# Kernel optimization log

Measured on AMD Instinct MI355X. Metric: run time of the kernel, lower is better.

## Reference

```python
import jax, jax.numpy as jnp
import numpy as np


def _avgpool2(x):
    # 2x2 average pool, stride 2, NHWC
    B, H, W, C = x.shape
    return x.reshape(B, H // 2, 2, W // 2, 2, C).mean(axis=(2, 4))


def setup_inputs() -> dict:
    key = jax.random.key(0)
    ks = jax.random.split(key, 5)
    B, H, W, C = 8, 64, 64, 512
    s = 0.02
    return {
        "x": jax.random.normal(ks[0], (B, H, W, C), dtype=jnp.float32),
        "wf": jax.random.normal(ks[1], (C, C // 8), dtype=jnp.float32) * s,
        "wg": jax.random.normal(ks[2], (C, C // 8), dtype=jnp.float32) * s,
        "wh": jax.random.normal(ks[3], (C, C // 2), dtype=jnp.float32) * s,
        "wo": jax.random.normal(ks[4], (C // 2, C), dtype=jnp.float32) * s,
    }


def reference(x, wf, wg, wh, wo):
    B, H, W, C = x.shape
    # queries from full resolution: 1x1 conv == channel matmul
    f = jnp.einsum("bhwc,cd->bhwd", x, wf).reshape(B, H * W, C // 8)
    # keys/values from 2x2 average-pooled map
    xp = _avgpool2(x)  # [B, H/2, W/2, C]
    g = jnp.einsum("bhwc,cd->bhwd", xp, wg).reshape(B, H * W // 4, C // 8)
    h = jnp.einsum("bhwc,cd->bhwd", xp, wh).reshape(B, H * W // 4, C // 2)
    # attn: [B, HW, HW/4], softmax over pooled key axis
    attn = jax.nn.softmax(jnp.einsum("bnd,bmd->bnm", f, g), axis=-1)
    y = jnp.einsum("bnm,bmd->bnd", attn, h).reshape(B, H, W, C // 2)
    # output 1x1 conv back to C channels
    return jnp.einsum("bhwc,cd->bhwd", y, wo)
```

## Files before the change

kernel.cpp:

```cpp
#include <hip/hip_runtime.h>
#include <hip/hip_bf16.h>

typedef __attribute__((ext_vector_type(8))) short bshort8;
typedef __attribute__((ext_vector_type(4))) float f32x4;
typedef __attribute__((ext_vector_type(4))) float vfloat4;
typedef __attribute__((ext_vector_type(4))) unsigned int vuint4;
typedef __attribute__((ext_vector_type(2))) unsigned int vuint2;

__device__ __forceinline__ unsigned short f2bf(float f) {
    union { float f; unsigned u; } v; v.f = f;
    unsigned u = v.u;
    u += 0x7fffu + ((u >> 16) & 1u);
    return (unsigned short)(u >> 16);
}

template<int EPI>
__global__ __launch_bounds__(256)
void gemm_bt(const unsigned short* __restrict__ Av, const unsigned short* __restrict__ Btv,
             void* __restrict__ Cv,
             int M, int N, int K,
             long long aB, long long bB, long long cB)
{
    __shared__ __align__(128) char sA[64 * 64];
    __shared__ __align__(128) char sB[64 * 64];

    const int b    = blockIdx.z;
    const int tid  = threadIdx.x;
    const int bRow = blockIdx.y << 6;
    const int bCol = blockIdx.x << 6;
    const int wid  = tid >> 6, lane = tid & 63;
    const int wr   = wid >> 1, wc   = wid & 1;
    const int r16  = lane & 15, kg  = lane >> 4;
    const int srow = tid >> 2,  skc = tid & 3;

    const unsigned short* A  = Av  + (size_t)aB * b;
    const unsigned short* Bt = Btv + (size_t)bB * b;

    f32x4 acc[2][2] = {};

    const size_t aRowBase = (size_t)(bRow + srow) * K + skc * 8;
    const size_t bRowBase = (size_t)(bCol + srow) * K + skc * 8;
    const unsigned swW = ((((unsigned)srow) << 6) | (((unsigned)skc) << 4))
                         ^ ((((unsigned)srow) & 7u) << 4);

    for (int k0 = 0; k0 < K; k0 += 32) {
        vuint4 apack = *(const vuint4*)(A  + aRowBase + k0);
        vuint4 bpack = *(const vuint4*)(Bt + bRowBase + k0);
        *(vuint4*)(sA + swW) = apack;
        *(vuint4*)(sB + swW) = bpack;
        __syncthreads();

        bshort8 af[2], bfr[2];
        #pragma unroll
        for (int mi = 0; mi < 2; mi++) {
            unsigned row = (unsigned)(wr * 32 + mi * 16 + r16);
            unsigned off = ((row << 6) | (((unsigned)kg) << 4)) ^ ((row & 7u) << 4);
            af[mi] = *(const bshort8*)(sA + off);
        }
        #pragma unroll
        for (int ni = 0; ni < 2; ni++) {
            unsigned col = (unsigned)(wc * 32 + ni * 16 + r16);
            unsigned off = ((col << 6) | (((unsigned)kg) << 4)) ^ ((col & 7u) << 4);
            bfr[ni] = *(const bshort8*)(sB + off);
        }
        #pragma unroll
        for (int mi = 0; mi < 2; mi++)
            #pragma unroll
            for (int ni = 0; ni < 2; ni++)
                acc[mi][ni] = __builtin_amdgcn_mfma_f32_16x16x32_bf16(
                                  af[mi], bfr[ni], acc[mi][ni], 0, 0, 0);
        __syncthreads();
    }

    #pragma unroll
    for (int mi = 0; mi < 2; mi++) {
        const int row0 = bRow + wr * 32 + mi * 16 + kg * 4;
        #pragma unroll
        for (int ni = 0; ni < 2; ni++) {
            const int col = bCol + wc * 32 + ni * 16 + r16;
            #pragma unroll
            for (int r = 0; r < 4; r++) {
                const int row = row0 + r;
                float x = acc[mi][ni][r];
                const size_t ci = (size_t)cB * b + (size_t)row * N + col;
                if constexpr (EPI == 0) ((float*)Cv)[ci] = x;
                else                    ((unsigned short*)Cv)[ci] = f2bf(x);
            }
        }
    }
}

__global__ __launch_bounds__(512)
void flash_attn(const float* __restrict__ x,
                const unsigned short* __restrict__ wft,
                const unsigned short* __restrict__ gb,
                const unsigned short* __restrict__ ht,
                unsigned short* __restrict__ yb)
{
    __shared__ __align__(128) char sS[128 * 128];
    __shared__ __align__(128) char sG[2][64 * 128];
    __shared__ __align__(128) char sH[2][256 * 128];
    __shared__ float rs[128];

    const int tid = threadIdx.x;
    const int bid = blockIdx.x;
    const int b   = bid & 7;
    const int q0  = (bid >> 3) << 7;
    const int wid = tid >> 6, lane = tid & 63;
    const int wr  = wid >> 1, wc = wid & 1;
    const int r16 = lane & 15, kg = lane >> 4;

    const float*          xB = x  + ((size_t)b * 4096 + q0) * 512;
    const unsigned short* gB = gb + (size_t)b * 1024 * 64;
    const unsigned short* hB = ht + (size_t)b * 256 * 1024;

    char* const sG0 = sG[0];
    char* const sH0 = sH[0];

    f32x4 facc[4] = {};
    {
        const int xrow = tid >> 2, xc = tid & 3;
        const int wrow = tid >> 3, wkc = tid & 7;
        const int frow = wid << 4;
        for (int k0 = 0; k0 < 512; k0 += 64) {
            {
                const float* p = xB + (size_t)xrow * 512 + k0 + xc * 16;
                #pragma unroll
                for (int j = 0; j < 2; j++) {
                    vfloat4 a0 = *(const vfloat4*)(p + j * 8);
                    vfloat4 a1 = *(const vfloat4*)(p + j * 8 + 4);
                    vuint4 w;
                    w[0] = (unsigned)f2bf(a0[0]) | ((unsigned)f2bf(a0[1]) << 16);
                    w[1] = (unsigned)f2bf(a0[2]) | ((unsigned)f2bf(a0[3]) << 16);
                    w[2] = (unsigned)f2bf(a1[0]) | ((unsigned)f2bf(a1[1]) << 16);
                    w[3] = (unsigned)f2bf(a1[2]) | ((unsigned)f2bf(a1[3]) << 16);
                    unsigned off = ((unsigned)xrow * 128 + (unsigned)(xc * 32 + j * 16))
                                   ^ (((unsigned)xrow & 7u) << 4);
                    *(vuint4*)(sH0 + off) = w;
                }
            }
            {
                vuint4 v = *(const vuint4*)(wft + (size_t)wrow * 512 + k0 + wkc * 8);
                unsigned off = ((unsigned)wrow * 128 + (unsigned)wkc * 16)
                               ^ (((unsigned)wrow & 7u) << 4);
                *(vuint4*)(sG0 + off) = v;
            }
            __syncthreads();

            bshort8 ax[2];
            {
                unsigned row = (unsigned)(frow + r16);
                unsigned base = row * 128, sw = (row & 7u) << 4;
                ax[0] = *(const bshort8*)(sH0 + ((base + (unsigned)kg * 16) ^ sw));
                ax[1] = *(const bshort8*)(sH0 + ((base + 64 + (unsigned)kg * 16) ^ sw));
            }
            #pragma unroll
            for (int ni = 0; ni < 4; ni++) {
                unsigned col = (unsigned)(ni * 16 + r16);
                unsigned base = col * 128, sw = (col & 7u) << 4;
                bshort8 b0 = *(const bshort8*)(sG0 + ((base + (unsigned)kg * 16) ^ sw));
                bshort8 b1 = *(const bshort8*)(sG0 + ((base + 64 + (unsigned)kg * 16) ^ sw));
                facc[ni] = __builtin_amdgcn_mfma_f32_16x16x32_bf16(ax[0], b0, facc[ni], 0, 0, 0);
                facc[ni] = __builtin_amdgcn_mfma_f32_16x16x32_bf16(ax[1], b1, facc[ni], 0, 0, 0);
            }
            __syncthreads();
        }

        const int frow2 = wid << 4;
        #pragma unroll
        for (int ni = 0; ni < 4; ni++) {
            const unsigned col = (unsigned)(ni * 16 + r16);
            #pragma unroll
            for (int r = 0; r < 4; r++) {
                unsigned row = (unsigned)(frow2 + kg * 4 + r);
                unsigned off = (row * 128 + col * 2) ^ ((row & 7u) << 4);
                *(unsigned short*)(sS + off) = f2bf(facc[ni][r]);
            }
        }
    }

    const int kc = tid & 7, n0 = tid >> 3;
    const unsigned gOff  = ((unsigned)n0 * 128 + (unsigned)kc * 16) ^ (((unsigned)n0 & 7u) << 4);
    const unsigned hOff0 = gOff;

    vuint4 gR, hR0, hR1, hR2, hR3;
    gR  = *(const vuint4*)(gB + (size_t)n0 * 64 + kc * 8);
    hR0 = *(const vuint4*)(hB + (size_t)(n0      ) * 1024 + kc * 8);
    hR1 = *(const vuint4*)(hB + (size_t)(n0 +  64) * 1024 + kc * 8);
    hR2 = *(const vuint4*)(hB + (size_t)(n0 + 128) * 1024 + kc * 8);
    hR3 = *(const vuint4*)(hB + (size_t)(n0 + 192) * 1024 + kc * 8);
    *(vuint4*)(sG0 + gOff)               = gR;
    *(vuint4*)(sH0 + hOff0)              = hR0;
    *(vuint4*)(sH0 + hOff0 +     8192)   = hR1;
    *(vuint4*)(sH0 + hOff0 + 2 * 8192)   = hR2;
    *(vuint4*)(sH0 + hOff0 + 3 * 8192)   = hR3;
    __syncthreads();

    bshort8 af[2][2];
    #pragma unroll
    for (int mi = 0; mi < 2; mi++) {
        unsigned row = (unsigned)(wr * 32 + mi * 16 + r16);
        unsigned base = row * 128, sw = (row & 7u) << 4;
        af[mi][0] = *(const bshort8*)(sS + ((base + (unsigned)kg * 16) ^ sw));
        af[mi][1] = *(const bshort8*)(sS + ((base + 64 + (unsigned)kg * 16) ^ sw));
    }
    __syncthreads();

    f32x4 yacc[2][8] = {};
    float psum[2][4] = {};

    for (int c = 0; c < 16; c++) {
        const int cur = c & 1;
        char* const sGc = sG[cur];
        char* const sHc = sH[cur];

        if (c < 15) {
            const int kv1 = (c + 1) << 6;
            gR  = *(const vuint4*)(gB + (size_t)(kv1 + n0) * 64 + kc * 8);
            hR0 = *(const vuint4*)(hB + (size_t)(n0      ) * 1024 + kv1 + kc * 8);
            hR1 = *(const vuint4*)(hB + (size_t)(n0 +  64) * 1024 + kv1 + kc * 8);
            hR2 = *(const vuint4*)(hB + (size_t)(n0 + 128) * 1024 + kv1 + kc * 8);
            hR3 = *(const vuint4*)(hB + (size_t)(n0 + 192) * 1024 + kv1 + kc * 8);
        }

        f32x4 sacc[2][2] = {};
        #pragma unroll
        for (int ni = 0; ni < 2; ni++) {
            unsigned col = (unsigned)(wc * 32 + ni * 16 + r16);
            unsigned base = col * 128, sw = (col & 7u) << 4;
            bshort8 g0 = *(const bshort8*)(sGc + ((base + (unsigned)kg * 16) ^ sw));
            bshort8 g1 = *(const bshort8*)(sGc + ((base + 64 + (unsigned)kg * 16) ^ sw));
            #pragma unroll
            for (int mi = 0; mi < 2; mi++) {
                sacc[mi][ni] = __builtin_amdgcn_mfma_f32_16x16x32_bf16(af[mi][0], g0, sacc[mi][ni], 0, 0, 0);
                sacc[mi][ni] = __builtin_amdgcn_mfma_f32_16x16x32_bf16(af[mi][1], g1, sacc[mi][ni], 0, 0, 0);
            }
        }

        #pragma unroll
        for (int mi = 0; mi < 2; mi++)
            #pragma unroll
            for (int ni = 0; ni < 2; ni++) {
                const unsigned col = (unsigned)(wc * 32 + ni * 16 + r16);
                #pragma unroll
                for (int r = 0; r < 4; r++) {
                    float e = __expf(sacc[mi][ni][r]);
                    psum[mi][r] += e;
                    unsigned row = (unsigned)(wr * 32 + mi * 16 + kg * 4 + r);
                    unsigned off = (row * 128 + col * 2) ^ ((row & 7u) << 4);
                    *(unsigned short*)(sS + off) = f2bf(e);
                }
            }
        __syncthreads();

        bshort8 pa[2][2];
        #pragma unroll
        for (int mi = 0; mi < 2; mi++) {
            unsigned row = (unsigned)(wr * 32 + mi * 16 + r16);
            unsigned base = row * 128, sw = (row & 7u) << 4;
            pa[mi][0] = *(const bshort8*)(sS + ((base + (unsigned)kg * 16) ^ sw));
            pa[mi][1] = *(const bshort8*)(sS + ((base + 64 + (unsigned)kg * 16) ^ sw));
        }
        #pragma unroll
        for (int ni = 0; ni < 8; ni++) {
            unsigned col = (unsigned)(wc * 128 + ni * 16 + r16);
            unsigned base = col * 128, sw = (col & 7u) << 4;
            bshort8 b0 = *(const bshort8*)(sHc + ((base + (unsigned)kg * 16) ^ sw));
            bshort8 b1 = *(const bshort8*)(sHc + ((base + 64 + (unsigned)kg * 16) ^ sw));
            #pragma unroll
            for (int mi = 0; mi < 2; mi++) {
                yacc[mi][ni] = __builtin_amdgcn_mfma_f32_16x16x32_bf16(pa[mi][0], b0, yacc[mi][ni], 0, 0, 0);
                yacc[mi][ni] = __builtin_amdgcn_mfma_f32_16x16x32_bf16(pa[mi][1], b1, yacc[mi][ni], 0, 0, 0);
            }
        }

        if (c < 15) {
            char* const sGn = sG[cur ^ 1];
            char* const sHn = sH[cur ^ 1];
            *(vuint4*)(sGn + gOff)             = gR;
            *(vuint4*)(sHn + hOff0)            = hR0;
            *(vuint4*)(sHn + hOff0 +     8192) = hR1;
            *(vuint4*)(sHn + hOff0 + 2 * 8192) = hR2;
            *(vuint4*)(sHn + hOff0 + 3 * 8192) = hR3;
        }
        __syncthreads();
    }

    #pragma unroll
    for (int mi = 0; mi < 2; mi++)
        #pragma unroll
        for (int r = 0; r < 4; r++) {
            float s = psum[mi][r];
            s += __shfl_xor(s, 1, 64);
            s += __shfl_xor(s, 2, 64);
            s += __shfl_xor(s, 4, 64);
            s += __shfl_xor(s, 8, 64);
            psum[mi][r] = s;
        }
    if (wc == 0 && r16 == 0) {
        #pragma unroll
        for (int mi = 0; mi < 2; mi++)
            #pragma unroll
            for (int r = 0; r < 4; r++)
                rs[wr * 32 + mi * 16 + kg * 4 + r] = psum[mi][r];
    }
    __syncthreads();
    if (wc == 1 && r16 == 0) {
        #pragma unroll
        for (int mi = 0; mi < 2; mi++)
            #pragma unroll
            for (int r = 0; r < 4; r++)
                rs[wr * 32 + mi * 16 + kg * 4 + r] += psum[mi][r];
    }
    __syncthreads();

    unsigned short* yB = yb + ((size_t)b * 4096 + q0) * 256;
    #pragma unroll
    for (int mi = 0; mi < 2; mi++)
        #pragma unroll
        for (int r = 0; r < 4; r++) {
            const int row = wr * 32 + mi * 16 + kg * 4 + r;
            const float rinv = 1.0f / rs[row];
            #pragma unroll
            for (int ni = 0; ni < 8; ni++) {
                const int col = wc * 128 + ni * 16 + r16;
                yB[(size_t)row * 256 + col] = f2bf(yacc[mi][ni][r] * rinv);
            }
        }
}

__global__ __launch_bounds__(256)
void pool2(const float* __restrict__ x, unsigned short* __restrict__ xp)
{
    const int t  = blockIdx.x * 256 + threadIdx.x;
    const int c4 = t & 127;
    const int j  = (t >> 7) & 31;
    const int i  = (t >> 12) & 31;
    const int b  = t >> 17;
    const float* p = x + ((((size_t)b * 64 + 2 * i) * 64) + 2 * j) * 512 + c4 * 4;
    vfloat4 a0 = *(const vfloat4*)p;
    vfloat4 a1 = *(const vfloat4*)(p + 512);
    vfloat4 a2 = *(const vfloat4*)(p + 64 * 512);
    vfloat4 a3 = *(const vfloat4*)(p + 64 * 512 + 512);
    float r0 = 0.25f * (a0[0] + a1[0] + a2[0] + a3[0]);
    float r1 = 0.25f * (a0[1] + a1[1] + a2[1] + a3[1]);
    float r2 = 0.25f * (a0[2] + a1[2] + a2[2] + a3[2]);
    float r3 = 0.25f * (a0[3] + a1[3] + a2[3] + a3[3]);
    vuint2 o;
    o[0] = (unsigned)f2bf(r0) | ((unsigned)f2bf(r1) << 16);
    o[1] = (unsigned)f2bf(r2) | ((unsigned)f2bf(r3) << 16);
    *(vuint2*)(xp + (size_t)t * 4) = o;
}

__global__ __launch_bounds__(256)
void wprep(const float* __restrict__ wf, const float* __restrict__ wg,
           const float* __restrict__ wh, const float* __restrict__ wo,
           unsigned short* __restrict__ wf_t, unsigned short* __restrict__ wg_t,
           unsigned short* __restrict__ wh_t, unsigned short* __restrict__ wo_t)
{
    __shared__ float tile[32][33];
    int t = blockIdx.x;
    const float* in; unsigned short* out; int K, N;
    if (t < 32)       { in = wf; out = wf_t; K = 512; N = 64;  }
    else if (t < 64)  { in = wg; out = wg_t; K = 512; N = 64;  t -= 32;  }
    else if (t < 192) { in = wh; out = wh_t; K = 512; N = 256; t -= 64;  }
    else              { in = wo; out = wo_t; K = 256; N = 512; t -= 192; }
    const int ntN = N >> 5;
    const int tk = (t / ntN) << 5, tn = (t % ntN) << 5;
    const int tx = threadIdx.x & 31, ty = threadIdx.x >> 5;
    #pragma unroll
    for (int s = 0; s < 4; s++)
        tile[ty + s * 8][tx] = in[(size_t)(tk + ty + s * 8) * N + tn + tx];
    __syncthreads();
    #pragma unroll
    for (int s = 0; s < 4; s++)
        out[(size_t)(tn + ty + s * 8) * K + tk + tx] = f2bf(tile[tx][ty + s * 8]);
}

extern "C" void kernel_launch(void* const* d_in, const int* in_sizes, int n_in,
                              void* d_out, int out_size, void* d_ws, size_t ws_size,
                              hipStream_t stream)
{
    const float* x  = (const float*)d_in[0];
    const float* wf = (const float*)d_in[1];
    const float* wg = (const float*)d_in[2];
    const float* wh = (const float*)d_in[3];
    const float* wo = (const float*)d_in[4];
    float* out = (float*)d_out;

    char* ws = (char*)d_ws;
    size_t off = 0;
    auto carve = [&](size_t bytes) {
        char* p = ws + off;
        off = (off + bytes + 255) & ~(size_t)255;
        return p;
    };
    unsigned short* xp   = (unsigned short*)carve(8ll * 1024 * 512 * 2);
    unsigned short* wf_t = (unsigned short*)carve(64 * 512 * 2);
    unsigned short* wg_t = (unsigned short*)carve(64 * 512 * 2);
    unsigned short* wh_t = (unsigned short*)carve(256 * 512 * 2);
    unsigned short* wo_t = (unsigned short*)carve(512 * 256 * 2);
    unsigned short* gb   = (unsigned short*)carve(8ll * 1024 * 64 * 2);
    unsigned short* ht   = (unsigned short*)carve(8ll * 256 * 1024 * 2);
    unsigned short* yb   = (unsigned short*)carve(8ll * 4096 * 256 * 2);

    wprep<<<dim3(320), 256, 0, stream>>>(wf, wg, wh, wo, wf_t, wg_t, wh_t, wo_t);

    pool2<<<dim3(4096), 256, 0, stream>>>(x, xp);

    gemm_bt<1><<<dim3(1, 128, 1), 256, 0, stream>>>(xp, wg_t, gb, 8192, 64, 512, 0, 0, 0);
    gemm_bt<1><<<dim3(16, 4, 8), 256, 0, stream>>>(wh_t, xp, ht, 256, 1024, 512,
                                                   0, 1024LL * 512, 256LL * 1024);

    flash_attn<<<dim3(256), 512, 0, stream>>>(x, wf_t, gb, ht, yb);

    gemm_bt<0><<<dim3(8, 512, 1), 256, 0, stream>>>(yb, wo_t, out, 32768, 512, 256, 0, 0, 0);
}
```

Before: 203.3 us.

## Give each wave its own 16 query rows to drop intra-loop barriers

Each of the 8 waves now owns 16 full query rows instead of a 32x(half-key/half-value) tile. The score matrix is computed transposed (G as the A operand), so the exp'd probabilities land in per-wave LDS scratch that only that wave reads. This removes one block-wide barrier per KV chunk and the cross-wave row-sum reduction through shared memory. It also adds s_setprio around MFMA sections. In exchange each wave reads all 256 H columns from LDS and holds 16 accumulators, which raises LDS traffic for B fragments and register pressure.

```diff
diff --git a/kernel.cpp b/kernel.cpp
--- a/kernel.cpp
+++ b/kernel.cpp
@@ -100,14 +100,12 @@
     __shared__ __align__(128) char sS[128 * 128];
     __shared__ __align__(128) char sG[2][64 * 128];
     __shared__ __align__(128) char sH[2][256 * 128];
-    __shared__ float rs[128];
 
     const int tid = threadIdx.x;
     const int bid = blockIdx.x;
     const int b   = bid & 7;
     const int q0  = (bid >> 3) << 7;
     const int wid = tid >> 6, lane = tid & 63;
-    const int wr  = wid >> 1, wc = wid & 1;
     const int r16 = lane & 15, kg = lane >> 4;
 
     const float*          xB = x  + ((size_t)b * 4096 + q0) * 512;
@@ -196,18 +194,16 @@
     *(vuint4*)(sH0 + hOff0 + 3 * 8192)   = hR3;
     __syncthreads();
 
-    bshort8 af[2][2];
-    #pragma unroll
-    for (int mi = 0; mi < 2; mi++) {
-        unsigned row = (unsigned)(wr * 32 + mi * 16 + r16);
-        unsigned base = row * 128, sw = (row & 7u) << 4;
-        af[mi][0] = *(const bshort8*)(sS + ((base + (unsigned)kg * 16) ^ sw));
-        af[mi][1] = *(const bshort8*)(sS + ((base + 64 + (unsigned)kg * 16) ^ sw));
-    }
-    __syncthreads();
-
-    f32x4 yacc[2][8] = {};
-    float psum[2][4] = {};
+    char* const sP = sS + (wid << 11);
+    bshort8 af[2];
+    {
+        unsigned base = (unsigned)r16 * 128, sw = ((unsigned)r16 & 7u) << 4;
+        af[0] = *(const bshort8*)(sP + ((base + (unsigned)kg * 16) ^ sw));
+        af[1] = *(const bshort8*)(sP + ((base + 64 + (unsigned)kg * 16) ^ sw));
+    }
+
+    f32x4 yacc[16] = {};
+    float psum = 0.f;
 
     for (int c = 0; c < 16; c++) {
         const int cur = c & 1;
@@ -223,56 +219,53 @@
             hR3 = *(const vuint4*)(hB + (size_t)(n0 + 192) * 1024 + kv1 + kc * 8);
         }
 
-        f32x4 sacc[2][2] = {};
-        #pragma unroll
-        for (int ni = 0; ni < 2; ni++) {
-            unsigned col = (unsigned)(wc * 32 + ni * 16 + r16);
-            unsigned base = col * 128, sw = (col & 7u) << 4;
-            bshort8 g0 = *(const bshort8*)(sGc + ((base + (unsigned)kg * 16) ^ sw));
-            bshort8 g1 = *(const bshort8*)(sGc + ((base + 64 + (unsigned)kg * 16) ^ sw));
-            #pragma unroll
-            for (int mi = 0; mi < 2; mi++) {
-                sacc[mi][ni] = __builtin_amdgcn_mfma_f32_16x16x32_bf16(af[mi][0], g0, sacc[mi][ni], 0, 0, 0);
-                sacc[mi][ni] = __builtin_amdgcn_mfma_f32_16x16x32_bf16(af[mi][1], g1, sacc[mi][ni], 0, 0, 0);
-            }
-        }
-
-        #pragma unroll
-        for (int mi = 0; mi < 2; mi++)
-            #pragma unroll
-            for (int ni = 0; ni < 2; ni++) {
-                const unsigned col = (unsigned)(wc * 32 + ni * 16 + r16);
-                #pragma unroll
-                for (int r = 0; r < 4; r++) {
-                    float e = __expf(sacc[mi][ni][r]);
-                    psum[mi][r] += e;
-                    unsigned row = (unsigned)(wr * 32 + mi * 16 + kg * 4 + r);
-                    unsigned off = (row * 128 + col * 2) ^ ((row & 7u) << 4);
-                    *(unsigned short*)(sS + off) = f2bf(e);
-                }
-            }
-        __syncthreads();
-
-        bshort8 pa[2][2];
-        #pragma unroll
-        for (int mi = 0; mi < 2; mi++) {
-            unsigned row = (unsigned)(wr * 32 + mi * 16 + r16);
-            unsigned base = row * 128, sw = (row & 7u) << 4;
-            pa[mi][0] = *(const bshort8*)(sS + ((base + (unsigned)kg * 16) ^ sw));
-            pa[mi][1] = *(const bshort8*)(sS + ((base + 64 + (unsigned)kg * 16) ^ sw));
-        }
-        #pragma unroll
-        for (int ni = 0; ni < 8; ni++) {
-            unsigned col = (unsigned)(wc * 128 + ni * 16 + r16);
+        f32x4 sacc[4] = {};
+        {
+            __builtin_amdgcn_s_setprio(1);
+            #pragma unroll
+            for (int kt = 0; kt < 4; kt++) {
+                unsigned row = (unsigned)(kt * 16 + r16);
+                unsigned base = row * 128, sw = (row & 7u) << 4;
+                bshort8 g0 = *(const bshort8*)(sGc + ((base + (unsigned)kg * 16) ^ sw));
+                bshort8 g1 = *(const bshort8*)(sGc + ((base + 64 + (unsigned)kg * 16) ^ sw));
+                sacc[kt] = __builtin_amdgcn_mfma_f32_16x16x32_bf16(g0, af[0], sacc[kt], 0, 0, 0);
+                sacc[kt] = __builtin_amdgcn_mfma_f32_16x16x32_bf16(g1, af[1], sacc[kt], 0, 0, 0);
+            }
+            __builtin_amdgcn_s_setprio(0);
+        }
+
+        #pragma unroll
+        for (int kt = 0; kt < 4; kt++) {
+            float e0 = __expf(sacc[kt][0]);
+            float e1 = __expf(sacc[kt][1]);
+            float e2 = __expf(sacc[kt][2]);
+            float e3 = __expf(sacc[kt][3]);
+            psum += (e0 + e1) + (e2 + e3);
+            vuint2 pk;
+            pk[0] = (unsigned)f2bf(e0) | ((unsigned)f2bf(e1) << 16);
+            pk[1] = (unsigned)f2bf(e2) | ((unsigned)f2bf(e3) << 16);
+            unsigned off = ((unsigned)r16 * 128 + (unsigned)(kt * 32 + kg * 8))
+                           ^ (((unsigned)r16 & 7u) << 4);
+            *(vuint2*)(sP + off) = pk;
+        }
+
+        bshort8 pa0, pa1;
+        {
+            unsigned base = (unsigned)r16 * 128, sw = ((unsigned)r16 & 7u) << 4;
+            pa0 = *(const bshort8*)(sP + ((base + (unsigned)kg * 16) ^ sw));
+            pa1 = *(const bshort8*)(sP + ((base + 64 + (unsigned)kg * 16) ^ sw));
+        }
+        __builtin_amdgcn_s_setprio(1);
+        #pragma unroll
+        for (int ni = 0; ni < 16; ni++) {
+            unsigned col = (unsigned)(ni * 16 + r16);
             unsigned base = col * 128, sw = (col & 7u) << 4;
             bshort8 b0 = *(const bshort8*)(sHc + ((base + (unsigned)kg * 16) ^ sw));
             bshort8 b1 = *(const bshort8*)(sHc + ((base + 64 + (unsigned)kg * 16) ^ sw));
-            #pragma unroll
-            for (int mi = 0; mi < 2; mi++) {
-                yacc[mi][ni] = __builtin_amdgcn_mfma_f32_16x16x32_bf16(pa[mi][0], b0, yacc[mi][ni], 0, 0, 0);
-                yacc[mi][ni] = __builtin_amdgcn_mfma_f32_16x16x32_bf16(pa[mi][1], b1, yacc[mi][ni], 0, 0, 0);
-            }
-        }
+            yacc[ni] = __builtin_amdgcn_mfma_f32_16x16x32_bf16(pa0, b0, yacc[ni], 0, 0, 0);
+            yacc[ni] = __builtin_amdgcn_mfma_f32_16x16x32_bf16(pa1, b1, yacc[ni], 0, 0, 0);
+        }
+        __builtin_amdgcn_s_setprio(0);
 
         if (c < 15) {
             char* const sGn = sG[cur ^ 1];
@@ -286,47 +279,24 @@
         __syncthreads();
     }
 
-    #pragma unroll
-    for (int mi = 0; mi < 2; mi++)
-        #pragma unroll
-        for (int r = 0; r < 4; r++) {
-            float s = psum[mi][r];
-            s += __shfl_xor(s, 1, 64);
-            s += __shfl_xor(s, 2, 64);
-            s += __shfl_xor(s, 4, 64);
-            s += __shfl_xor(s, 8, 64);
-            psum[mi][r] = s;
-        }
-    if (wc == 0 && r16 == 0) {
-        #pragma unroll
-        for (int mi = 0; mi < 2; mi++)
-            #pragma unroll
-            for (int r = 0; r < 4; r++)
-                rs[wr * 32 + mi * 16 + kg * 4 + r] = psum[mi][r];
-    }
-    __syncthreads();
-    if (wc == 1 && r16 == 0) {
-        #pragma unroll
-        for (int mi = 0; mi < 2; mi++)
-            #pragma unroll
-            for (int r = 0; r < 4; r++)
-                rs[wr * 32 + mi * 16 + kg * 4 + r] += psum[mi][r];
-    }
-    __syncthreads();
-
-    unsigned short* yB = yb + ((size_t)b * 4096 + q0) * 256;
-    #pragma unroll
-    for (int mi = 0; mi < 2; mi++)
-        #pragma unroll
-        for (int r = 0; r < 4; r++) {
-            const int row = wr * 32 + mi * 16 + kg * 4 + r;
-            const float rinv = 1.0f / rs[row];
-            #pragma unroll
-            for (int ni = 0; ni < 8; ni++) {
-                const int col = wc * 128 + ni * 16 + r16;
-                yB[(size_t)row * 256 + col] = f2bf(yacc[mi][ni][r] * rinv);
-            }
-        }
+    psum += __shfl_xor(psum, 16, 64);
+    psum += __shfl_xor(psum, 32, 64);
+    const float rinv = 1.0f / psum;
+
+    unsigned short* yB = yb + ((size_t)b * 4096 + q0 + wid * 16) * 256;
+    float rv[4];
+    #pragma unroll
+    for (int r = 0; r < 4; r++)
+        rv[r] = __shfl(rinv, kg * 4 + r, 16);
+    #pragma unroll
+    for (int r = 0; r < 4; r++) {
+        const int row = kg * 4 + r;
+        #pragma unroll
+        for (int ni = 0; ni < 16; ni++) {
+            const int col = ni * 16 + r16;
+            yB[(size_t)row * 256 + col] = f2bf(yacc[ni][r] * rv[r]);
+        }
+    }
 }
 
 __global__ __launch_bounds__(256)
```

Result: no change. 204.1 us (+0.4%).
